# Kernel optimization log

Hardware: AMD Instinct MI355X
Metric: run time of the kernel (lower is better)

Reference implementation:

```python
import jax, jax.numpy as jnp
import numpy as np

B, S, D, H = 2, 2048, 1024, 16
DK = D // H


def setup_inputs() -> dict:
    key = jax.random.key(0)
    ks = jax.random.split(key, 11)
    s = 1.0 / np.sqrt(D)
    inp = {
        "q": jax.random.normal(ks[0], (B, S, D), jnp.float32),
        "k": jax.random.normal(ks[1], (B, S, D), jnp.float32),
        "v": jax.random.normal(ks[2], (B, S, D), jnp.float32),
        "mask": jnp.tril(jnp.ones((S, S), jnp.int32))[None, None],  # causal [1,1,S,S]
        "w_q": jax.random.normal(ks[3], (D, D), jnp.float32) * s,
        "b_q": jax.random.normal(ks[4], (D,), jnp.float32) * 0.01,
        "w_k": jax.random.normal(ks[5], (D, D), jnp.float32) * s,
        "b_k": jax.random.normal(ks[6], (D,), jnp.float32) * 0.01,
        "w_v": jax.random.normal(ks[7], (D, D), jnp.float32) * s,
        "b_v": jax.random.normal(ks[8], (D,), jnp.float32) * 0.01,
        "w_o": jax.random.normal(ks[9], (D, D), jnp.float32) * s,
        "b_o": jax.random.normal(ks[10], (D,), jnp.float32) * 0.01,
    }
    return inp


def reference(q, k, v, mask, w_q, b_q, w_k, b_k, w_v, b_v, w_o, b_o):
    # Linear projections (torch Linear: x @ W.T + b)
    query = q @ w_q.T + b_q  # [B,S,D]
    key_ = k @ w_k.T + b_k
    value = v @ w_v.T + b_v
    # split heads -> [B,H,S,DK]
    def split(x):
        return x.reshape(B, S, H, DK).transpose(0, 2, 1, 3)
    qh, kh, vh = split(query), split(key_), split(value)
    scores = jnp.einsum("bhqd,bhkd->bhqk", qh, kh) / jnp.sqrt(jnp.float32(DK))
    scores = jnp.where(mask == 0, jnp.float32(-1e9), scores)
    attn = jax.nn.softmax(scores, axis=-1)
    out = jnp.einsum("bhqk,bhkd->bhqd", attn, vh)  # [B,H,S,DK]
    out = out.transpose(0, 2, 1, 3).reshape(B, S, D)
    return out @ w_o.T + b_o
```

## Files before the change

### kernel.cpp

```cpp
#include <hip/hip_runtime.h>


typedef __attribute__((ext_vector_type(8))) short bf16x8;
typedef __attribute__((ext_vector_type(4))) float floatx4;
typedef __attribute__((ext_vector_type(4))) unsigned short u16x4;

#define S_LEN 2048
#define D_MODEL 1024
#define N_HEADS 16
#define D_HEAD 64
#define M_ROWS 4096
#define QSCALE 0.18033688011112042f

#define XSTR 1088
#define VSTR 4160

__device__ __forceinline__ unsigned short f32_to_bf16(float f) {
  unsigned int u = __builtin_bit_cast(unsigned int, f);
  u += 0x7FFFu + ((u >> 16) & 1u);
  return (unsigned short)(u >> 16);
}

__device__ __forceinline__ void async_lds16(const unsigned short* g, unsigned short* l) {
  __builtin_amdgcn_global_load_lds(
      (const __attribute__((address_space(1))) unsigned int*)g,
      (__attribute__((address_space(3))) unsigned int*)l, 16, 0, 0);
}

__global__ __launch_bounds__(256) void cvt_w(
    const float* __restrict__ w0, const float* __restrict__ w1,
    const float* __restrict__ w2, const float* __restrict__ w3,
    unsigned short* __restrict__ dst) {
  const int row = blockIdx.x;
  const int z = blockIdx.y;
  const float* src = ((z == 0) ? w0 : (z == 1) ? w1 : (z == 2) ? w2 : w3) + (long)row * 1024;
  unsigned short* d = dst + (long)z * 1024 * XSTR + (long)row * XSTR;
  const int tid = threadIdx.x;
  float4 f = ((const float4*)src)[tid];
  u16x4 o;
  o[0] = f32_to_bf16(f.x); o[1] = f32_to_bf16(f.y);
  o[2] = f32_to_bf16(f.z); o[3] = f32_to_bf16(f.w);
  *(u16x4*)(d + tid * 4) = o;
}

__global__ __launch_bounds__(256) void cvt_x(
    const float* __restrict__ x0, const float* __restrict__ x1,
    const float* __restrict__ x2, unsigned short* __restrict__ dst) {
  const int row = blockIdx.x;
  const int z = blockIdx.y;
  const float* src = ((z == 0) ? x0 : (z == 1) ? x1 : x2) + (long)row * 1024;
  unsigned short* d = dst + (long)z * M_ROWS * XSTR + (long)row * XSTR;
  const int tid = threadIdx.x;
  float4 f = ((const float4*)src)[tid];
  u16x4 o;
  o[0] = f32_to_bf16(f.x); o[1] = f32_to_bf16(f.y);
  o[2] = f32_to_bf16(f.z); o[3] = f32_to_bf16(f.w);
  *(u16x4*)(d + tid * 4) = o;
}

#define GK 1024
#define GN 1024

template <bool XPRE>
__global__ __launch_bounds__(256, 3) void qkv_gemm(
    const float* __restrict__ Xq, const float* __restrict__ Xk, const float* __restrict__ Xv,
    const unsigned short* __restrict__ Xb,
    const unsigned short* __restrict__ Wb,
    const float* __restrict__ bq, const float* __restrict__ bk, const float* __restrict__ bv,
    unsigned short* __restrict__ Yq, unsigned short* __restrict__ Yk,
    unsigned short* __restrict__ Yvt) {
  __shared__ __align__(16) unsigned short As[128 * 64];
  __shared__ __align__(16) unsigned short Bs[128 * 64];

  const int z = blockIdx.z;
  const unsigned short* W = Wb + (long)z * 1024 * XSTR;
  const float* bias = (z == 0) ? bq : ((z == 1) ? bk : bv);

  const int r0 = blockIdx.x * 128;
  const int n0 = blockIdx.y * 128;
  const int tid = threadIdx.x;
  const int lane = tid & 63;
  const int wave = tid >> 6;
  const int quad = lane >> 4;
  const int ln = lane & 15;
  const int wm = (wave >> 1) * 64;
  const int wn = (wave & 1) * 64;

  floatx4 acc[4][4];
#pragma unroll
  for (int i = 0; i < 4; i++)
#pragma unroll
    for (int j = 0; j < 4; j++) acc[i][j] = (floatx4){0.f, 0.f, 0.f, 0.f};

  const int srow = (lane >> 3);
  const int scol8 = (lane & 7) * 8;
  const unsigned short* ApH = nullptr;
  const float* ApF = nullptr;
  if constexpr (XPRE) {
    ApH = Xb + (long)z * M_ROWS * XSTR;
  } else {
    ApF = (z == 0) ? Xq : ((z == 1) ? Xk : Xv);
  }

  for (int k0 = 0; k0 < GK; k0 += 64) {
    __syncthreads();
    if constexpr (XPRE) {
#pragma unroll
      for (int i = 0; i < 4; i++) {
        const int row = wave * 32 + i * 8;
        async_lds16(ApH + (long)(r0 + row + srow) * XSTR + k0 + scol8,
                    As + row * 64);
        async_lds16(W + (long)(n0 + row + srow) * XSTR + k0 + scol8,
                    Bs + row * 64);
      }
    } else {
      const int arow = tid >> 1;
      const int acol = (tid & 1) * 32;
      unsigned short ua[32] __attribute__((aligned(16)));
      float fa[32] __attribute__((aligned(16)));
#pragma unroll
      for (int c = 0; c < 8; c++)
        *(float4*)(fa + c * 4) = *(const float4*)(ApF + (long)(r0 + arow) * GK + k0 + acol + c * 4);
#pragma unroll
      for (int j = 0; j < 32; j++) ua[j] = f32_to_bf16(fa[j]);
      *(float4*)(As + arow * 64 + acol) = *(float4*)(ua);
      *(float4*)(As + arow * 64 + acol + 8) = *(float4*)(ua + 8);
      *(float4*)(As + arow * 64 + acol + 16) = *(float4*)(ua + 16);
      *(float4*)(As + arow * 64 + acol + 24) = *(float4*)(ua + 24);
#pragma unroll
      for (int i = 0; i < 4; i++) {
        const int row = wave * 32 + i * 8;
        async_lds16(W + (long)(n0 + row + srow) * XSTR + k0 + scol8,
                    Bs + row * 64);
      }
    }
    __syncthreads();

#pragma unroll
    for (int ks = 0; ks < 64; ks += 32) {
      bf16x8 af[4], bfr[4];
#pragma unroll
      for (int mt = 0; mt < 4; mt++)
        af[mt] = *(const bf16x8*)(As + (wm + mt * 16 + ln) * 64 + ks + quad * 8);
#pragma unroll
      for (int nt = 0; nt < 4; nt++)
        bfr[nt] = *(const bf16x8*)(Bs + (wn + nt * 16 + ln) * 64 + ks + quad * 8);
#pragma unroll
      for (int mt = 0; mt < 4; mt++)
#pragma unroll
        for (int nt = 0; nt < 4; nt++)
          acc[mt][nt] = __builtin_amdgcn_mfma_f32_16x16x32_bf16(af[mt], bfr[nt], acc[mt][nt], 0, 0, 0);
    }
  }

#pragma unroll
  for (int nt = 0; nt < 4; nt++) {
    const int n = n0 + wn + nt * 16 + ln;
    const float bv = bias[n];
#pragma unroll
    for (int mt = 0; mt < 4; mt++) {
      const int r = r0 + wm + mt * 16 + quad * 4;
      if (z == 2) {
        u16x4 pk;
#pragma unroll
        for (int reg = 0; reg < 4; reg++) pk[reg] = f32_to_bf16(acc[mt][nt][reg] + bv);
        *(u16x4*)(Yvt + (long)n * VSTR + r) = pk;
      } else if (z == 0) {
#pragma unroll
        for (int reg = 0; reg < 4; reg++)
          Yq[(long)(r + reg) * XSTR + n] = f32_to_bf16((acc[mt][nt][reg] + bv) * QSCALE);
      } else {
#pragma unroll
        for (int reg = 0; reg < 4; reg++)
          Yk[(long)(r + reg) * XSTR + n] = f32_to_bf16(acc[mt][nt][reg] + bv);
      }
    }
  }
}

__global__ __launch_bounds__(256, 3) void out_gemm(
    const unsigned short* __restrict__ X,
    const unsigned short* __restrict__ W,
    const float* __restrict__ bias,
    float* __restrict__ Y) {
  __shared__ __align__(16) unsigned short As[64 * 64];
  __shared__ __align__(16) unsigned short Bs[128 * 64];

  const int r0 = blockIdx.x * 64;
  const int n0 = blockIdx.y * 128;
  const int tid = threadIdx.x;
  const int lane = tid & 63;
  const int wave = tid >> 6;
  const int quad = lane >> 4;
  const int ln = lane & 15;
  const int wm = (wave >> 1) * 32;
  const int wn = (wave & 1) * 64;

  floatx4 acc[2][4];
#pragma unroll
  for (int i = 0; i < 2; i++)
#pragma unroll
    for (int j = 0; j < 4; j++) acc[i][j] = (floatx4){0.f, 0.f, 0.f, 0.f};

  const int srow = (lane >> 3);
  const int scol8 = (lane & 7) * 8;

  for (int k0 = 0; k0 < GK; k0 += 64) {
    __syncthreads();
#pragma unroll
    for (int i = 0; i < 2; i++) {
      const int row = wave * 16 + i * 8;
      async_lds16(X + (long)(r0 + row + srow) * XSTR + k0 + scol8, As + row * 64);
    }
#pragma unroll
    for (int i = 0; i < 4; i++) {
      const int row = wave * 32 + i * 8;
      async_lds16(W + (long)(n0 + row + srow) * XSTR + k0 + scol8, Bs + row * 64);
    }
    __syncthreads();

#pragma unroll
    for (int ks = 0; ks < 64; ks += 32) {
      bf16x8 af[2], bfr[4];
#pragma unroll
      for (int mt = 0; mt < 2; mt++)
        af[mt] = *(const bf16x8*)(As + (wm + mt * 16 + ln) * 64 + ks + quad * 8);
#pragma unroll
      for (int nt = 0; nt < 4; nt++)
        bfr[nt] = *(const bf16x8*)(Bs + (wn + nt * 16 + ln) * 64 + ks + quad * 8);
#pragma unroll
      for (int mt = 0; mt < 2; mt++)
#pragma unroll
        for (int nt = 0; nt < 4; nt++)
          acc[mt][nt] = __builtin_amdgcn_mfma_f32_16x16x32_bf16(af[mt], bfr[nt], acc[mt][nt], 0, 0, 0);
    }
  }

#pragma unroll
  for (int nt = 0; nt < 4; nt++) {
    const int n = n0 + wn + nt * 16 + ln;
    const float bv = bias[n];
#pragma unroll
    for (int mt = 0; mt < 2; mt++) {
      const int r = r0 + wm + mt * 16 + quad * 4;
#pragma unroll
      for (int reg = 0; reg < 4; reg++)
        Y[(long)(r + reg) * GN + n] = acc[mt][nt][reg] + bv;
    }
  }
}

#define PSTR 72

__global__ __launch_bounds__(64, 2) void attn_causal(
    const unsigned short* __restrict__ Q,
    const unsigned short* __restrict__ K,
    const unsigned short* __restrict__ Vt,
    unsigned short* __restrict__ O) {
  __shared__ __align__(16) unsigned short PbA[16 * PSTR];
  __shared__ __align__(16) unsigned short PbB[16 * PSTR];

  const int bh = blockIdx.x;
  const int pr = blockIdx.y;
  const int b = bh >> 4;
  const int h = bh & 15;

  const int lane = threadIdx.x;
  const int quad = lane >> 4;
  const int ln = lane & 15;

  const int s1 = pr, s2 = 127 - pr;
  const int q0A = s1 * 16, q0B = s2 * 16;
  const int nkt1 = (s1 >> 2) + 1;
  const int nkt2 = (s2 >> 2) + 1;

  const unsigned short* Qb = Q + (long)b * S_LEN * XSTR + h * D_HEAD;
  const unsigned short* Kb = K + (long)b * S_LEN * XSTR + h * D_HEAD;
  const unsigned short* Vb = Vt + (long)h * D_HEAD * VSTR + b * S_LEN;

  bf16x8 qfA[2], qfB[2];
  qfA[0] = *(const bf16x8*)(Qb + (long)(q0A + ln) * XSTR + quad * 8);
  qfA[1] = *(const bf16x8*)(Qb + (long)(q0A + ln) * XSTR + 32 + quad * 8);
  qfB[0] = *(const bf16x8*)(Qb + (long)(q0B + ln) * XSTR + quad * 8);
  qfB[1] = *(const bf16x8*)(Qb + (long)(q0B + ln) * XSTR + 32 + quad * 8);

  float mA = -1e30f, lA = 0.f, mB = -1e30f, lB = 0.f;
  floatx4 oA[4], oB[4];
#pragma unroll
  for (int nt = 0; nt < 4; nt++) {
    oA[nt] = (floatx4){0.f, 0.f, 0.f, 0.f};
    oB[nt] = (floatx4){0.f, 0.f, 0.f, 0.f};
  }

  auto loadKV = [&](bf16x8 (&kf)[4][2], bf16x8 (&vf)[4][2], int kt) {
    const int kv0 = kt * 64;
#pragma unroll
    for (int ct = 0; ct < 4; ct++) {
      const unsigned short* kp = Kb + (long)(kv0 + ct * 16 + ln) * XSTR + quad * 8;
      kf[ct][0] = *(const bf16x8*)(kp);
      kf[ct][1] = *(const bf16x8*)(kp + 32);
      const unsigned short* vp = Vb + (long)(ct * 16 + ln) * VSTR + kv0 + quad * 8;
      vf[ct][0] = *(const bf16x8*)(vp);
      vf[ct][1] = *(const bf16x8*)(vp + 32);
    }
  };

  auto iter = [&](bf16x8 (&kf)[4][2], bf16x8 (&vf)[4][2], int kt) {
    const int kv0 = kt * 64;
    const bool aAct = (kt < nkt1);

    floatx4 sB[4], sA[4];
#pragma unroll
    for (int ct = 0; ct < 4; ct++) {
      sB[ct] = (floatx4){0.f, 0.f, 0.f, 0.f};
      sB[ct] = __builtin_amdgcn_mfma_f32_16x16x32_bf16(kf[ct][0], qfB[0], sB[ct], 0, 0, 0);
      sB[ct] = __builtin_amdgcn_mfma_f32_16x16x32_bf16(kf[ct][1], qfB[1], sB[ct], 0, 0, 0);
    }
    if (aAct) {
#pragma unroll
      for (int ct = 0; ct < 4; ct++) {
        sA[ct] = (floatx4){0.f, 0.f, 0.f, 0.f};
        sA[ct] = __builtin_amdgcn_mfma_f32_16x16x32_bf16(kf[ct][0], qfA[0], sA[ct], 0, 0, 0);
        sA[ct] = __builtin_amdgcn_mfma_f32_16x16x32_bf16(kf[ct][1], qfA[1], sA[ct], 0, 0, 0);
      }
    }

    {
      float tmax = -1e30f;
      if (kt == nkt2 - 1) {
        const int qg = q0B + ln;
#pragma unroll
        for (int ct = 0; ct < 4; ct++) {
          const int kvb = kv0 + ct * 16 + quad * 4;
#pragma unroll
          for (int reg = 0; reg < 4; reg++) {
            float sv = sB[ct][reg];
            if (kvb + reg > qg) sv = -1e30f;
            sB[ct][reg] = sv;
            tmax = fmaxf(tmax, sv);
          }
        }
      } else {
#pragma unroll
        for (int ct = 0; ct < 4; ct++)
#pragma unroll
          for (int reg = 0; reg < 4; reg++) tmax = fmaxf(tmax, sB[ct][reg]);
      }
      tmax = fmaxf(tmax, __shfl_xor(tmax, 16, 64));
      tmax = fmaxf(tmax, __shfl_xor(tmax, 32, 64));
      const float mnew = fmaxf(mB, tmax);
      const float alpha = exp2f(mB - mnew);
      mB = mnew;
      float rsum = 0.f;
#pragma unroll
      for (int ct = 0; ct < 4; ct++) {
        u16x4 pk;
#pragma unroll
        for (int reg = 0; reg < 4; reg++) {
          const float p = exp2f(sB[ct][reg] - mB);
          rsum += p;
          pk[reg] = f32_to_bf16(p);
        }
        *(u16x4*)(PbB + ln * PSTR + ct * 16 + quad * 4) = pk;
      }
      rsum += __shfl_xor(rsum, 16, 64);
      rsum += __shfl_xor(rsum, 32, 64);
      lB = lB * alpha + rsum;
#pragma unroll
      for (int nt = 0; nt < 4; nt++)
#pragma unroll
        for (int reg = 0; reg < 4; reg++) oB[nt][reg] *= alpha;
    }

    if (aAct) {
      float tmax = -1e30f;
      if (kt == nkt1 - 1) {
        const int qg = q0A + ln;
#pragma unroll
        for (int ct = 0; ct < 4; ct++) {
          const int kvb = kv0 + ct * 16 + quad * 4;
#pragma unroll
          for (int reg = 0; reg < 4; reg++) {
            float sv = sA[ct][reg];
            if (kvb + reg > qg) sv = -1e30f;
            sA[ct][reg] = sv;
            tmax = fmaxf(tmax, sv);
          }
        }
      } else {
#pragma unroll
        for (int ct = 0; ct < 4; ct++)
#pragma unroll
          for (int reg = 0; reg < 4; reg++) tmax = fmaxf(tmax, sA[ct][reg]);
      }
      tmax = fmaxf(tmax, __shfl_xor(tmax, 16, 64));
      tmax = fmaxf(tmax, __shfl_xor(tmax, 32, 64));
      const float mnew = fmaxf(mA, tmax);
      const float alpha = exp2f(mA - mnew);
      mA = mnew;
      float rsum = 0.f;
#pragma unroll
      for (int ct = 0; ct < 4; ct++) {
        u16x4 pk;
#pragma unroll
        for (int reg = 0; reg < 4; reg++) {
          const float p = exp2f(sA[ct][reg] - mA);
          rsum += p;
          pk[reg] = f32_to_bf16(p);
        }
        *(u16x4*)(PbA + ln * PSTR + ct * 16 + quad * 4) = pk;
      }
      rsum += __shfl_xor(rsum, 16, 64);
      rsum += __shfl_xor(rsum, 32, 64);
      lA = lA * alpha + rsum;
#pragma unroll
      for (int nt = 0; nt < 4; nt++)
#pragma unroll
        for (int reg = 0; reg < 4; reg++) oA[nt][reg] *= alpha;
    }

    __builtin_amdgcn_wave_barrier();

    {
      bf16x8 p0 = *(const bf16x8*)(PbB + ln * PSTR + quad * 8);
      bf16x8 p1 = *(const bf16x8*)(PbB + ln * PSTR + 32 + quad * 8);
#pragma unroll
      for (int nt = 0; nt < 4; nt++) {
        oB[nt] = __builtin_amdgcn_mfma_f32_16x16x32_bf16(vf[nt][0], p0, oB[nt], 0, 0, 0);
        oB[nt] = __builtin_amdgcn_mfma_f32_16x16x32_bf16(vf[nt][1], p1, oB[nt], 0, 0, 0);
      }
    }
    if (aAct) {
      bf16x8 p0 = *(const bf16x8*)(PbA + ln * PSTR + quad * 8);
      bf16x8 p1 = *(const bf16x8*)(PbA + ln * PSTR + 32 + quad * 8);
#pragma unroll
      for (int nt = 0; nt < 4; nt++) {
        oA[nt] = __builtin_amdgcn_mfma_f32_16x16x32_bf16(vf[nt][0], p0, oA[nt], 0, 0, 0);
        oA[nt] = __builtin_amdgcn_mfma_f32_16x16x32_bf16(vf[nt][1], p1, oA[nt], 0, 0, 0);
      }
    }
    __builtin_amdgcn_wave_barrier();
  };

  bf16x8 kf0[4][2], vf0[4][2], kf1[4][2], vf1[4][2];
  loadKV(kf0, vf0, 0);
#pragma unroll 1
  for (int kt = 0; kt < nkt2; kt += 2) {
    if (kt + 1 < nkt2) loadKV(kf1, vf1, kt + 1);
    iter(kf0, vf0, kt);
    if (kt + 1 >= nkt2) break;
    if (kt + 2 < nkt2) loadKV(kf0, vf0, kt + 2);
    iter(kf1, vf1, kt + 1);
  }

  {
    const float inv = 1.0f / lA;
    unsigned short* op = O + (long)b * S_LEN * XSTR + (long)(q0A + ln) * XSTR + h * D_HEAD;
#pragma unroll
    for (int nt = 0; nt < 4; nt++) {
      u16x4 pk;
#pragma unroll
      for (int reg = 0; reg < 4; reg++) pk[reg] = f32_to_bf16(oA[nt][reg] * inv);
      *(u16x4*)(op + nt * 16 + quad * 4) = pk;
    }
  }
  {
    const float inv = 1.0f / lB;
    unsigned short* op = O + (long)b * S_LEN * XSTR + (long)(q0B + ln) * XSTR + h * D_HEAD;
#pragma unroll
    for (int nt = 0; nt < 4; nt++) {
      u16x4 pk;
#pragma unroll
      for (int reg = 0; reg < 4; reg++) pk[reg] = f32_to_bf16(oB[nt][reg] * inv);
      *(u16x4*)(op + nt * 16 + quad * 4) = pk;
    }
  }
}

extern "C" void kernel_launch(void* const* d_in, const int* in_sizes, int n_in,
                              void* d_out, int out_size, void* d_ws, size_t ws_size,
                              hipStream_t stream) {
  const float* q = (const float*)d_in[0];
  const float* k = (const float*)d_in[1];
  const float* v = (const float*)d_in[2];
  const float* w_q = (const float*)d_in[4];
  const float* b_q = (const float*)d_in[5];
  const float* w_k = (const float*)d_in[6];
  const float* b_k = (const float*)d_in[7];
  const float* w_v = (const float*)d_in[8];
  const float* b_v = (const float*)d_in[9];
  const float* w_o = (const float*)d_in[10];
  const float* b_o = (const float*)d_in[11];
  float* out = (float*)d_out;

  unsigned short* ws = (unsigned short*)d_ws;
  const long NR = (long)M_ROWS * XSTR;
  const long NV = (long)1024 * VSTR;
  const long NWALL = (long)4 * 1024 * XSTR;
  const long NXALL = 3 * NR;
  const long TOT_XPRE = 2 * NR + NV + NWALL + NXALL;
  const bool xpre = (ws_size >= (size_t)TOT_XPRE * sizeof(unsigned short));

  unsigned short *Qp, *Kp, *Vpt, *AO, *Wb, *Xb;
  if (xpre) {
    Qp = ws;
    Kp = ws + NR;
    Vpt = ws + 2 * NR;
    Wb = ws + 2 * NR + NV;
    Xb = Wb + NWALL;
    AO = Xb;
  } else {
    Qp = ws;
    Kp = ws + NR;
    Vpt = ws + 2 * NR;
    AO = ws + 2 * NR + NV;
    Wb = AO + NR;
    Xb = nullptr;
  }

  cvt_w<<<dim3(1024, 4), 256, 0, stream>>>(w_q, w_k, w_v, w_o, Wb);
  if (xpre) {
    cvt_x<<<dim3(4096, 3), 256, 0, stream>>>(q, k, v, Xb);
    qkv_gemm<true><<<dim3(M_ROWS / 128, GN / 128, 3), 256, 0, stream>>>(
        q, k, v, Xb, Wb, b_q, b_k, b_v, Qp, Kp, Vpt);
  } else {
    qkv_gemm<false><<<dim3(M_ROWS / 128, GN / 128, 3), 256, 0, stream>>>(
        q, k, v, nullptr, Wb, b_q, b_k, b_v, Qp, Kp, Vpt);
  }
  attn_causal<<<dim3(2 * N_HEADS, 64), 64, 0, stream>>>(Qp, Kp, Vpt, AO);
  out_gemm<<<dim3(M_ROWS / 64, GN / 128), 256, 0, stream>>>(AO, Wb + 3 * (long)1024 * XSTR, b_o, out);
}
```

Baseline: 282.5 us.

## Split paired-tile attention into one 16-row query tile per block with 32-wide KV steps

The causal attention kernel no longer pairs a short and a long query tile in one block. Each block now handles a single 16-row query tile, launching twice as many blocks ordered longest-first, and steps through keys in 32-wide chunks. The launch bound rises to allow more waves per SIMD through lower register use. The double-buffered register prefetch of K/V is dropped, so load latency must be hidden by occupancy instead, and the narrower KV step means more softmax rescale overhead per key.

```diff
diff --git a/kernel.cpp b/kernel.cpp
--- a/kernel.cpp
+++ b/kernel.cpp
@@ -250,18 +250,17 @@
   }
 }
 
-#define PSTR 72
-
-__global__ __launch_bounds__(64, 2) void attn_causal(
+#define PB_STR 40
+
+__global__ __launch_bounds__(64, 6) void attn_causal(
     const unsigned short* __restrict__ Q,
     const unsigned short* __restrict__ K,
     const unsigned short* __restrict__ Vt,
     unsigned short* __restrict__ O) {
-  __shared__ __align__(16) unsigned short PbA[16 * PSTR];
-  __shared__ __align__(16) unsigned short PbB[16 * PSTR];
-
-  const int bh = blockIdx.x;
-  const int pr = blockIdx.y;
+  __shared__ __align__(16) unsigned short Pb[16 * PB_STR];
+
+  const int s = 127 - blockIdx.x;
+  const int bh = blockIdx.y;
   const int b = bh >> 4;
   const int h = bh & 15;
 
@@ -269,212 +268,120 @@
   const int quad = lane >> 4;
   const int ln = lane & 15;
 
-  const int s1 = pr, s2 = 127 - pr;
-  const int q0A = s1 * 16, q0B = s2 * 16;
-  const int nkt1 = (s1 >> 2) + 1;
-  const int nkt2 = (s2 >> 2) + 1;
+  const int q0 = s * 16;
+  const int nkt = (s >> 1) + 1;
 
   const unsigned short* Qb = Q + (long)b * S_LEN * XSTR + h * D_HEAD;
   const unsigned short* Kb = K + (long)b * S_LEN * XSTR + h * D_HEAD;
   const unsigned short* Vb = Vt + (long)h * D_HEAD * VSTR + b * S_LEN;
 
-  bf16x8 qfA[2], qfB[2];
-  qfA[0] = *(const bf16x8*)(Qb + (long)(q0A + ln) * XSTR + quad * 8);
-  qfA[1] = *(const bf16x8*)(Qb + (long)(q0A + ln) * XSTR + 32 + quad * 8);
-  qfB[0] = *(const bf16x8*)(Qb + (long)(q0B + ln) * XSTR + quad * 8);
-  qfB[1] = *(const bf16x8*)(Qb + (long)(q0B + ln) * XSTR + 32 + quad * 8);
-
-  float mA = -1e30f, lA = 0.f, mB = -1e30f, lB = 0.f;
-  floatx4 oA[4], oB[4];
-#pragma unroll
-  for (int nt = 0; nt < 4; nt++) {
-    oA[nt] = (floatx4){0.f, 0.f, 0.f, 0.f};
-    oB[nt] = (floatx4){0.f, 0.f, 0.f, 0.f};
-  }
-
-  auto loadKV = [&](bf16x8 (&kf)[4][2], bf16x8 (&vf)[4][2], int kt) {
-    const int kv0 = kt * 64;
-#pragma unroll
-    for (int ct = 0; ct < 4; ct++) {
-      const unsigned short* kp = Kb + (long)(kv0 + ct * 16 + ln) * XSTR + quad * 8;
-      kf[ct][0] = *(const bf16x8*)(kp);
-      kf[ct][1] = *(const bf16x8*)(kp + 32);
-      const unsigned short* vp = Vb + (long)(ct * 16 + ln) * VSTR + kv0 + quad * 8;
-      vf[ct][0] = *(const bf16x8*)(vp);
-      vf[ct][1] = *(const bf16x8*)(vp + 32);
-    }
-  };
-
-  auto iter = [&](bf16x8 (&kf)[4][2], bf16x8 (&vf)[4][2], int kt) {
-    const int kv0 = kt * 64;
-    const bool aAct = (kt < nkt1);
-
-    floatx4 sB[4], sA[4];
-#pragma unroll
-    for (int ct = 0; ct < 4; ct++) {
-      sB[ct] = (floatx4){0.f, 0.f, 0.f, 0.f};
-      sB[ct] = __builtin_amdgcn_mfma_f32_16x16x32_bf16(kf[ct][0], qfB[0], sB[ct], 0, 0, 0);
-      sB[ct] = __builtin_amdgcn_mfma_f32_16x16x32_bf16(kf[ct][1], qfB[1], sB[ct], 0, 0, 0);
-    }
-    if (aAct) {
-#pragma unroll
-      for (int ct = 0; ct < 4; ct++) {
-        sA[ct] = (floatx4){0.f, 0.f, 0.f, 0.f};
-        sA[ct] = __builtin_amdgcn_mfma_f32_16x16x32_bf16(kf[ct][0], qfA[0], sA[ct], 0, 0, 0);
-        sA[ct] = __builtin_amdgcn_mfma_f32_16x16x32_bf16(kf[ct][1], qfA[1], sA[ct], 0, 0, 0);
+  bf16x8 qf0 = *(const bf16x8*)(Qb + (long)(q0 + ln) * XSTR + quad * 8);
+  bf16x8 qf1 = *(const bf16x8*)(Qb + (long)(q0 + ln) * XSTR + 32 + quad * 8);
+
+  float m = -1e30f, l = 0.f;
+  floatx4 o0 = (floatx4){0.f, 0.f, 0.f, 0.f};
+  floatx4 o1 = (floatx4){0.f, 0.f, 0.f, 0.f};
+  floatx4 o2 = (floatx4){0.f, 0.f, 0.f, 0.f};
+  floatx4 o3 = (floatx4){0.f, 0.f, 0.f, 0.f};
+
+  const unsigned short* kRow = Kb + (long)ln * XSTR + quad * 8;
+  const unsigned short* vRow = Vb + (long)ln * VSTR + quad * 8;
+
+#pragma unroll 1
+  for (int kt = 0; kt < nkt; kt++) {
+    const int kv0 = kt * 32;
+
+    bf16x8 k00 = *(const bf16x8*)(kRow + (long)kv0 * XSTR);
+    bf16x8 k01 = *(const bf16x8*)(kRow + (long)kv0 * XSTR + 32);
+    bf16x8 k10 = *(const bf16x8*)(kRow + (long)(kv0 + 16) * XSTR);
+    bf16x8 k11 = *(const bf16x8*)(kRow + (long)(kv0 + 16) * XSTR + 32);
+    floatx4 s0 = (floatx4){0.f, 0.f, 0.f, 0.f};
+    floatx4 s1 = (floatx4){0.f, 0.f, 0.f, 0.f};
+    s0 = __builtin_amdgcn_mfma_f32_16x16x32_bf16(k00, qf0, s0, 0, 0, 0);
+    s0 = __builtin_amdgcn_mfma_f32_16x16x32_bf16(k01, qf1, s0, 0, 0, 0);
+    s1 = __builtin_amdgcn_mfma_f32_16x16x32_bf16(k10, qf0, s1, 0, 0, 0);
+    s1 = __builtin_amdgcn_mfma_f32_16x16x32_bf16(k11, qf1, s1, 0, 0, 0);
+
+    bf16x8 v0 = *(const bf16x8*)(vRow + kv0);
+    bf16x8 v1 = *(const bf16x8*)(vRow + 16 * VSTR + kv0);
+    bf16x8 v2 = *(const bf16x8*)(vRow + 32 * VSTR + kv0);
+    bf16x8 v3 = *(const bf16x8*)(vRow + 48 * VSTR + kv0);
+
+    float tmax = -1e30f;
+    if (kt == nkt - 1) {
+      const int qg = q0 + ln;
+      const int kvb0 = kv0 + quad * 4;
+      const int kvb1 = kv0 + 16 + quad * 4;
+#pragma unroll
+      for (int reg = 0; reg < 4; reg++) {
+        float a = s0[reg];
+        if (kvb0 + reg > qg) a = -1e30f;
+        s0[reg] = a;
+        tmax = fmaxf(tmax, a);
+        float c = s1[reg];
+        if (kvb1 + reg > qg) c = -1e30f;
+        s1[reg] = c;
+        tmax = fmaxf(tmax, c);
       }
-    }
-
-    {
-      float tmax = -1e30f;
-      if (kt == nkt2 - 1) {
-        const int qg = q0B + ln;
-#pragma unroll
-        for (int ct = 0; ct < 4; ct++) {
-          const int kvb = kv0 + ct * 16 + quad * 4;
-#pragma unroll
-          for (int reg = 0; reg < 4; reg++) {
-            float sv = sB[ct][reg];
-            if (kvb + reg > qg) sv = -1e30f;
-            sB[ct][reg] = sv;
-            tmax = fmaxf(tmax, sv);
-          }
-        }
-      } else {
-#pragma unroll
-        for (int ct = 0; ct < 4; ct++)
-#pragma unroll
-          for (int reg = 0; reg < 4; reg++) tmax = fmaxf(tmax, sB[ct][reg]);
+    } else {
+#pragma unroll
+      for (int reg = 0; reg < 4; reg++) {
+        tmax = fmaxf(tmax, s0[reg]);
+        tmax = fmaxf(tmax, s1[reg]);
       }
-      tmax = fmaxf(tmax, __shfl_xor(tmax, 16, 64));
-      tmax = fmaxf(tmax, __shfl_xor(tmax, 32, 64));
-      const float mnew = fmaxf(mB, tmax);
-      const float alpha = exp2f(mB - mnew);
-      mB = mnew;
-      float rsum = 0.f;
-#pragma unroll
-      for (int ct = 0; ct < 4; ct++) {
-        u16x4 pk;
-#pragma unroll
-        for (int reg = 0; reg < 4; reg++) {
-          const float p = exp2f(sB[ct][reg] - mB);
-          rsum += p;
-          pk[reg] = f32_to_bf16(p);
-        }
-        *(u16x4*)(PbB + ln * PSTR + ct * 16 + quad * 4) = pk;
-      }
-      rsum += __shfl_xor(rsum, 16, 64);
-      rsum += __shfl_xor(rsum, 32, 64);
-      lB = lB * alpha + rsum;
-#pragma unroll
-      for (int nt = 0; nt < 4; nt++)
-#pragma unroll
-        for (int reg = 0; reg < 4; reg++) oB[nt][reg] *= alpha;
-    }
-
-    if (aAct) {
-      float tmax = -1e30f;
-      if (kt == nkt1 - 1) {
-        const int qg = q0A + ln;
-#pragma unroll
-        for (int ct = 0; ct < 4; ct++) {
-          const int kvb = kv0 + ct * 16 + quad * 4;
-#pragma unroll
-          for (int reg = 0; reg < 4; reg++) {
-            float sv = sA[ct][reg];
-            if (kvb + reg > qg) sv = -1e30f;
-            sA[ct][reg] = sv;
-            tmax = fmaxf(tmax, sv);
-          }
-        }
-      } else {
-#pragma unroll
-        for (int ct = 0; ct < 4; ct++)
-#pragma unroll
-          for (int reg = 0; reg < 4; reg++) tmax = fmaxf(tmax, sA[ct][reg]);
-      }
-      tmax = fmaxf(tmax, __shfl_xor(tmax, 16, 64));
-      tmax = fmaxf(tmax, __shfl_xor(tmax, 32, 64));
-      const float mnew = fmaxf(mA, tmax);
-      const float alpha = exp2f(mA - mnew);
-      mA = mnew;
-      float rsum = 0.f;
-#pragma unroll
-      for (int ct = 0; ct < 4; ct++) {
-        u16x4 pk;
-#pragma unroll
-        for (int reg = 0; reg < 4; reg++) {
-          const float p = exp2f(sA[ct][reg] - mA);
-          rsum += p;
-          pk[reg] = f32_to_bf16(p);
-        }
-        *(u16x4*)(PbA + ln * PSTR + ct * 16 + quad * 4) = pk;
-      }
-      rsum += __shfl_xor(rsum, 16, 64);
-      rsum += __shfl_xor(rsum, 32, 64);
-      lA = lA * alpha + rsum;
-#pragma unroll
-      for (int nt = 0; nt < 4; nt++)
-#pragma unroll
-        for (int reg = 0; reg < 4; reg++) oA[nt][reg] *= alpha;
+    }
+    tmax = fmaxf(tmax, __shfl_xor(tmax, 16, 64));
+    tmax = fmaxf(tmax, __shfl_xor(tmax, 32, 64));
+    const float mnew = fmaxf(m, tmax);
+    const float alpha = exp2f(m - mnew);
+    m = mnew;
+
+    float rsum = 0.f;
+    u16x4 pk0, pk1;
+#pragma unroll
+    for (int reg = 0; reg < 4; reg++) {
+      const float p0 = exp2f(s0[reg] - m);
+      rsum += p0;
+      pk0[reg] = f32_to_bf16(p0);
+      const float p1 = exp2f(s1[reg] - m);
+      rsum += p1;
+      pk1[reg] = f32_to_bf16(p1);
+    }
+    *(u16x4*)(Pb + ln * PB_STR + quad * 4) = pk0;
+    *(u16x4*)(Pb + ln * PB_STR + 16 + quad * 4) = pk1;
+    rsum += __shfl_xor(rsum, 16, 64);
+    rsum += __shfl_xor(rsum, 32, 64);
+    l = l * alpha + rsum;
+#pragma unroll
+    for (int reg = 0; reg < 4; reg++) {
+      o0[reg] *= alpha; o1[reg] *= alpha; o2[reg] *= alpha; o3[reg] *= alpha;
     }
 
     __builtin_amdgcn_wave_barrier();
 
-    {
-      bf16x8 p0 = *(const bf16x8*)(PbB + ln * PSTR + quad * 8);
-      bf16x8 p1 = *(const bf16x8*)(PbB + ln * PSTR + 32 + quad * 8);
-#pragma unroll
-      for (int nt = 0; nt < 4; nt++) {
-        oB[nt] = __builtin_amdgcn_mfma_f32_16x16x32_bf16(vf[nt][0], p0, oB[nt], 0, 0, 0);
-        oB[nt] = __builtin_amdgcn_mfma_f32_16x16x32_bf16(vf[nt][1], p1, oB[nt], 0, 0, 0);
-      }
-    }
-    if (aAct) {
-      bf16x8 p0 = *(const bf16x8*)(PbA + ln * PSTR + quad * 8);
-      bf16x8 p1 = *(const bf16x8*)(PbA + ln * PSTR + 32 + quad * 8);
-#pragma unroll
-      for (int nt = 0; nt < 4; nt++) {
-        oA[nt] = __builtin_amdgcn_mfma_f32_16x16x32_bf16(vf[nt][0], p0, oA[nt], 0, 0, 0);
-        oA[nt] = __builtin_amdgcn_mfma_f32_16x16x32_bf16(vf[nt][1], p1, oA[nt], 0, 0, 0);
-      }
-    }
+    bf16x8 p = *(const bf16x8*)(Pb + ln * PB_STR + quad * 8);
+    o0 = __builtin_amdgcn_mfma_f32_16x16x32_bf16(v0, p, o0, 0, 0, 0);
+    o1 = __builtin_amdgcn_mfma_f32_16x16x32_bf16(v1, p, o1, 0, 0, 0);
+    o2 = __builtin_amdgcn_mfma_f32_16x16x32_bf16(v2, p, o2, 0, 0, 0);
+    o3 = __builtin_amdgcn_mfma_f32_16x16x32_bf16(v3, p, o3, 0, 0, 0);
+
     __builtin_amdgcn_wave_barrier();
-  };
-
-  bf16x8 kf0[4][2], vf0[4][2], kf1[4][2], vf1[4][2];
-  loadKV(kf0, vf0, 0);
-#pragma unroll 1
-  for (int kt = 0; kt < nkt2; kt += 2) {
-    if (kt + 1 < nkt2) loadKV(kf1, vf1, kt + 1);
-    iter(kf0, vf0, kt);
-    if (kt + 1 >= nkt2) break;
-    if (kt + 2 < nkt2) loadKV(kf0, vf0, kt + 2);
-    iter(kf1, vf1, kt + 1);
-  }
-
-  {
-    const float inv = 1.0f / lA;
-    unsigned short* op = O + (long)b * S_LEN * XSTR + (long)(q0A + ln) * XSTR + h * D_HEAD;
-#pragma unroll
-    for (int nt = 0; nt < 4; nt++) {
-      u16x4 pk;
-#pragma unroll
-      for (int reg = 0; reg < 4; reg++) pk[reg] = f32_to_bf16(oA[nt][reg] * inv);
-      *(u16x4*)(op + nt * 16 + quad * 4) = pk;
-    }
-  }
-  {
-    const float inv = 1.0f / lB;
-    unsigned short* op = O + (long)b * S_LEN * XSTR + (long)(q0B + ln) * XSTR + h * D_HEAD;
-#pragma unroll
-    for (int nt = 0; nt < 4; nt++) {
-      u16x4 pk;
-#pragma unroll
-      for (int reg = 0; reg < 4; reg++) pk[reg] = f32_to_bf16(oB[nt][reg] * inv);
-      *(u16x4*)(op + nt * 16 + quad * 4) = pk;
-    }
-  }
+  }
+
+  const float inv = 1.0f / l;
+  unsigned short* op = O + (long)b * S_LEN * XSTR + (long)(q0 + ln) * XSTR + h * D_HEAD;
+  u16x4 w0, w1, w2, w3;
+#pragma unroll
+  for (int reg = 0; reg < 4; reg++) {
+    w0[reg] = f32_to_bf16(o0[reg] * inv);
+    w1[reg] = f32_to_bf16(o1[reg] * inv);
+    w2[reg] = f32_to_bf16(o2[reg] * inv);
+    w3[reg] = f32_to_bf16(o3[reg] * inv);
+  }
+  *(u16x4*)(op + quad * 4) = w0;
+  *(u16x4*)(op + 16 + quad * 4) = w1;
+  *(u16x4*)(op + 32 + quad * 4) = w2;
+  *(u16x4*)(op + 48 + quad * 4) = w3;
 }
 
 extern "C" void kernel_launch(void* const* d_in, const int* in_sizes, int n_in,
@@ -527,6 +434,6 @@
     qkv_gemm<false><<<dim3(M_ROWS / 128, GN / 128, 3), 256, 0, stream>>>(
         q, k, v, nullptr, Wb, b_q, b_k, b_v, Qp, Kp, Vpt);
   }
-  attn_causal<<<dim3(2 * N_HEADS, 64), 64, 0, stream>>>(Qp, Kp, Vpt, AO);
+  attn_causal<<<dim3(128, 32), 64, 0, stream>>>(Qp, Kp, Vpt, AO);
   out_gemm<<<dim3(M_ROWS / 64, GN / 128), 256, 0, stream>>>(AO, Wb + 3 * (long)1024 * XSTR, b_o, out);
 }
```

Measured after the change: 418.7 us. +48.2%, slower.
